# Kernel optimization log

Hardware: AMD Instinct MI355X
Metric: run time of the kernel (lower is better)

The kernel has to match this reference:

```python
import jax, jax.numpy as jnp
import numpy as np

N = 100000   # nodes per graph-batch side
E = 1280000  # directed edges
G = 256      # graphs per batch
F_IN, HID, EMB = 64, 128, 64
BN_EPS = 1e-5


def setup_inputs() -> dict:
    key = jax.random.key(0)
    ks = jax.random.split(key, 24)
    inp = {}
    inp["x1"] = jax.random.normal(ks[0], (N, F_IN), dtype=jnp.float32)
    inp["x2"] = jax.random.normal(ks[1], (N, F_IN), dtype=jnp.float32)
    inp["edge_index1"] = jax.random.randint(ks[2], (2, E), 0, N, dtype=jnp.int64)
    inp["edge_index2"] = jax.random.randint(ks[3], (2, E), 0, N, dtype=jnp.int64)
    inp["batch1"] = jnp.sort(jax.random.randint(ks[4], (N,), 0, G, dtype=jnp.int64))
    inp["batch2"] = jnp.sort(jax.random.randint(ks[5], (N,), 0, G, dtype=jnp.int64))
    # shared (siamese) encoder parameters: 3 GIN layers (Linear+BN), final linear
    dims = [(F_IN, HID), (HID, HID), (HID, HID)]
    for i, (di, do) in enumerate(dims, 1):
        inp[f"W{i}"] = jax.random.normal(ks[5 + i], (di, do), dtype=jnp.float32) * (1.0 / np.sqrt(di))
        inp[f"b{i}"] = jnp.zeros((do,), dtype=jnp.float32)
        inp[f"g{i}"] = jnp.ones((do,), dtype=jnp.float32)   # BN gamma
        inp[f"be{i}"] = jnp.zeros((do,), dtype=jnp.float32)  # BN beta
    inp["Wf"] = jax.random.normal(ks[10], (HID, EMB), dtype=jnp.float32) * (1.0 / np.sqrt(HID))
    inp["bf"] = jnp.zeros((EMB,), dtype=jnp.float32)
    # classifier: Linear(EMB, HID//2) -> ReLU -> Linear(HID//2, 1) -> Sigmoid
    inp["Wc1"] = jax.random.normal(ks[11], (EMB, HID // 2), dtype=jnp.float32) * (1.0 / np.sqrt(EMB))
    inp["bc1"] = jnp.zeros((HID // 2,), dtype=jnp.float32)
    inp["Wc2"] = jax.random.normal(ks[12], (HID // 2, 1), dtype=jnp.float32) * (1.0 / np.sqrt(HID // 2))
    inp["bc2"] = jnp.zeros((1,), dtype=jnp.float32)
    return inp


def _gin_layer(x, src, dst, W, b, g, be):
    # GINConv eps=0: agg = x + sum_{j->i} x_j ; MLP = Linear -> BatchNorm1d -> ReLU
    agg = x + jax.ops.segment_sum(x[src], dst, num_segments=N)
    h = agg @ W + b
    mu = jnp.mean(h, axis=0)
    var = jnp.var(h, axis=0)
    h = (h - mu) * jax.lax.rsqrt(var + BN_EPS) * g + be
    return jax.nn.relu(h)  # MLP ReLU; outer .relu() in forward is idempotent


def _encode(x, edge_index, batch, Ws, bs, gs, bes, Wf, bf):
    src, dst = edge_index[0], edge_index[1]
    for W, b, g, be in zip(Ws, bs, gs, bes):
        x = _gin_layer(x, src, dst, W, b, g, be)
    # global_mean_pool
    sums = jax.ops.segment_sum(x, batch, num_segments=G)
    cnt = jax.ops.segment_sum(jnp.ones((N,), x.dtype), batch, num_segments=G)
    pooled = sums / jnp.maximum(cnt, 1.0)[:, None]
    return pooled @ Wf + bf


def reference(x1, edge_index1, batch1, x2, edge_index2, batch2,
              W1, b1, g1, be1, W2, b2, g2, be2, W3, b3, g3, be3,
              Wf, bf, Wc1, bc1, Wc2, bc2):
    Ws, bs, gs, bes = (W1, W2, W3), (b1, b2, b3), (g1, g2, g3), (be1, be2, be3)
    v1 = _encode(x1, edge_index1, batch1, Ws, bs, gs, bes, Wf, bf)
    v2 = _encode(x2, edge_index2, batch2, Ws, bs, gs, bes, Wf, bf)
    diff = jnp.abs(v1 - v2)
    h = jax.nn.relu(diff @ Wc1 + bc1)
    return jax.nn.sigmoid(h @ Wc2 + bc2)  # [G, 1]
```

## Files before the change

kernel.cpp:

```cpp
#include <hip/hip_runtime.h>
#include <hip/hip_bf16.h>
#include <math.h>

#define NN 100000
#define NE 1280000
#define NG 256
#define HID 128
#define EMB 64
#define BN_EPS 1e-5f
#define SB 1024
#define SNB ((NN + SB - 1) / SB)
#define NBG 1563
#define NB4 25000
#define PART ((NN + 7) / 8)
#define FCH 2048
#define NCH (NE / FCH)

typedef __attribute__((ext_vector_type(8))) __bf16 bf16x8;
typedef __attribute__((ext_vector_type(4))) float f32x4;

__device__ __forceinline__ float bf2f(unsigned int u) { return __uint_as_float(u << 16); }
__device__ __forceinline__ unsigned int f2b(float f) {
    unsigned int u = __float_as_uint(f);
    return (u + 0x7fffu + ((u >> 16) & 1u)) >> 16;
}

__global__ void detect_i64_kernel(const void* __restrict__ ei, int* __restrict__ flag) {
    if (threadIdx.x == 0 && blockIdx.x == 0) {
        const unsigned long long* p = (const unsigned long long*)ei;
        int is64 = 1;
        #pragma unroll
        for (int i = 0; i < 16; ++i)
            if (p[i] >= (1ull << 32)) is64 = 0;
        *flag = is64;
    }
}

__device__ __forceinline__ int load_idx(const void* p, int i, bool is64) {
    return is64 ? (int)((const long long*)p)[i] : ((const int*)p)[i];
}

__global__ __launch_bounds__(256) void convert_x(const float* __restrict__ x1,
                                                 const float* __restrict__ x2,
                                                 ushort* __restrict__ o1,
                                                 ushort* __restrict__ o2) {
    const int per = NN * 16;
    const int i = blockIdx.x * 256 + threadIdx.x;
    const int side = i >= per;
    const int j = i - side * per;
    const float4 v = ((const float4*)(side ? x2 : x1))[j];
    ushort4 o;
    o.x = (ushort)f2b(v.x); o.y = (ushort)f2b(v.y);
    o.z = (ushort)f2b(v.z); o.w = (ushort)f2b(v.w);
    ((ushort4*)(side ? o2 : o1))[j] = o;
}

__global__ __launch_bounds__(256) void prep_weights(const float* __restrict__ W1,
                                                    const float* __restrict__ W2,
                                                    const float* __restrict__ W3,
                                                    ushort* __restrict__ T1,
                                                    ushort* __restrict__ T2,
                                                    ushort* __restrict__ T3) {
    const int i = blockIdx.x * 256 + threadIdx.x;
    if (i < 8192) {
        const int k = i >> 7, c = i & 127;
        T1[c * 64 + k] = (ushort)f2b(W1[i]);
    } else if (i < 24576) {
        const int j = i - 8192, k = j >> 7, c = j & 127;
        T2[c * 128 + k] = (ushort)f2b(W2[j]);
    } else if (i < 40960) {
        const int j = i - 24576, k = j >> 7, c = j & 127;
        T3[c * 128 + k] = (ushort)f2b(W3[j]);
    }
}

__global__ __launch_bounds__(256) void csr_hist2(const void* __restrict__ e1,
                                                 const void* __restrict__ e2,
                                                 int* __restrict__ degA,
                                                 int* __restrict__ degB,
                                                 const int* __restrict__ flag) {
    const bool is64 = (*flag != 0);
    const int i = blockIdx.x * 256 + threadIdx.x;
    if (i < 2 * NE) {
        const int side = i >= NE;
        const int j = i - side * NE;
        atomicAdd(&(side ? degB : degA)[load_idx(side ? e2 : e1, NE + j, is64)], 1);
    }
}

__global__ __launch_bounds__(256) void scan_block_sums2(const int* __restrict__ degA,
                                                        const int* __restrict__ degB,
                                                        int* __restrict__ bsum) {
    const int side = blockIdx.x >= SNB;
    const int bx = blockIdx.x - side * SNB;
    const int* deg = side ? degB : degA;
    const int t = threadIdx.x;
    const int base = bx * SB + t * 4;
    int s = 0;
    #pragma unroll
    for (int k = 0; k < 4; ++k) {
        const int i = base + k;
        if (i < NN) s += deg[i];
    }
    __shared__ int red[256];
    red[t] = s;
    __syncthreads();
    for (int off = 128; off > 0; off >>= 1) {
        if (t < off) red[t] += red[t + off];
        __syncthreads();
    }
    if (t == 0) bsum[side * 128 + bx] = red[0];
}

__global__ __launch_bounds__(128) void scan_bsums2(const int* __restrict__ bsum,
                                                   int* __restrict__ boff,
                                                   int* __restrict__ rpA,
                                                   int* __restrict__ rpB) {
    const int side = blockIdx.x;
    __shared__ int s[128];
    const int t = threadIdx.x;
    s[t] = (t < SNB) ? bsum[side * 128 + t] : 0;
    __syncthreads();
    for (int off = 1; off < 128; off <<= 1) {
        const int v = (t >= off) ? s[t - off] : 0;
        __syncthreads();
        s[t] += v;
        __syncthreads();
    }
    boff[side * 128 + t] = (t == 0) ? 0 : s[t - 1];
    if (t == 0) (side ? rpB : rpA)[NN] = s[SNB - 1];
}

__global__ __launch_bounds__(256) void scan_fill2(const int* __restrict__ degA,
                                                  const int* __restrict__ degB,
                                                  const int* __restrict__ boff,
                                                  int* __restrict__ rpA,
                                                  int* __restrict__ rpB,
                                                  int* __restrict__ curA,
                                                  int* __restrict__ curB) {
    const int side = blockIdx.x >= SNB;
    const int bx = blockIdx.x - side * SNB;
    const int* deg = side ? degB : degA;
    int* rowptr = side ? rpB : rpA;
    int* cursor = side ? curB : curA;
    const int t = threadIdx.x;
    const int base = bx * SB + t * 4;
    int v[4], s = 0;
    #pragma unroll
    for (int k = 0; k < 4; ++k) {
        const int i = base + k;
        v[k] = (i < NN) ? deg[i] : 0;
        s += v[k];
    }
    __shared__ int red[256];
    red[t] = s;
    __syncthreads();
    for (int off = 1; off < 256; off <<= 1) {
        const int x = (t >= off) ? red[t - off] : 0;
        __syncthreads();
        red[t] += x;
        __syncthreads();
    }
    int run = boff[side * 128 + bx] + ((t == 0) ? 0 : red[t - 1]);
    #pragma unroll
    for (int k = 0; k < 4; ++k) {
        const int i = base + k;
        if (i < NN) {
            rowptr[i] = run;
            cursor[i] = run;
            run += v[k];
        }
    }
}

__global__ __launch_bounds__(256) void csr_fill_part(const void* __restrict__ e1,
                                                     const void* __restrict__ e2,
                                                     int* __restrict__ curA,
                                                     int* __restrict__ curB,
                                                     int* __restrict__ colA,
                                                     int* __restrict__ colB,
                                                     const int* __restrict__ flag) {
    const bool is64 = (*flag != 0);
    const int g = blockIdx.x & 7;
    const int q = blockIdx.x >> 3;
    const int side = q >= NCH;
    const int chunk = q - side * NCH;
    const void* __restrict__ e = side ? e2 : e1;
    int* __restrict__ cur = side ? curB : curA;
    int* __restrict__ col = side ? colB : colA;
    const int lo = g * PART;
    const int hi = min(lo + PART, NN);
    const int base = chunk * FCH;
    for (int i = base + threadIdx.x; i < base + FCH; i += 256) {
        const int d = load_idx(e, NE + i, is64);
        if (d >= lo && d < hi) {
            const int pos = atomicAdd(&cur[d], 1);
            col[pos] = load_idx(e, i, is64);
        }
    }
}

struct G64Args {
    const ushort *xA, *xB;
    const int *rpA, *rpB, *colA, *colB;
    ushort *oA, *oB;
};

__global__ __launch_bounds__(256) void gather64k(G64Args a) {
    const int xcd = blockIdx.x & 7;
    const int side = xcd >> 2;
    const int bx = (blockIdx.x >> 3) * 4 + (xcd & 3);
    const ushort* __restrict__ x = side ? a.xB : a.xA;
    const int* __restrict__ rowptr = side ? a.rpB : a.rpA;
    const int* __restrict__ col = side ? a.colB : a.colA;
    ushort* __restrict__ out = side ? a.oB : a.oA;

    const int node = (bx * 256 + threadIdx.x) >> 6;
    const int lane = threadIdx.x & 63;
    if (node >= NN) return;
    const int beg = rowptr[node], end = rowptr[node + 1];
    float acc = bf2f(x[node * 64 + lane]);
    int e = beg;
    for (; e + 3 < end; e += 4) {
        const int s0 = col[e], s1 = col[e + 1], s2 = col[e + 2], s3 = col[e + 3];
        acc += bf2f(x[s0 * 64 + lane]) + bf2f(x[s1 * 64 + lane])
             + bf2f(x[s2 * 64 + lane]) + bf2f(x[s3 * 64 + lane]);
    }
    for (; e < end; ++e) acc += bf2f(x[col[e] * 64 + lane]);
    out[node * 64 + lane] = (ushort)f2b(acc);
}

struct GPostArgs {
    const ushort *yA, *yB;
    const int *rpA, *rpB, *colA, *colB;
    ushort *rA, *rB;
    float *stA, *stB;
};

__global__ __launch_bounds__(256) void gather_post(GPostArgs a) {
    const int xcd = blockIdx.x & 7;
    const int side = xcd >> 2;
    const int bx = (blockIdx.x >> 3) * 4 + (xcd & 3);
    if (bx >= NBG) return;
    const ushort* __restrict__ y = side ? a.yB : a.yA;
    const int* __restrict__ rowptr = side ? a.rpB : a.rpA;
    const int* __restrict__ col = side ? a.colB : a.colA;
    ushort* __restrict__ r = side ? a.rB : a.rA;
    float* __restrict__ stats = side ? a.stB : a.stA;

    const int t = threadIdx.x;
    const int w = t >> 6, l = t & 63;
    const int c2 = l * 2;
    float s0 = 0.f, s1 = 0.f, q0 = 0.f, q1 = 0.f;

    for (int i = 0; i < 16; ++i) {
        const int node = bx * 64 + w * 16 + i;
        if (node >= NN) break;
        const int beg = rowptr[node], end = rowptr[node + 1];
        const unsigned int u0 = *(const unsigned int*)&y[(size_t)node * 128 + c2];
        float ax = bf2f(u0 & 0xffffu), ay = bf2f(u0 >> 16);
        int e = beg;
        for (; e + 3 < end; e += 4) {
            const int sa = col[e], sb = col[e + 1], sc = col[e + 2], sd = col[e + 3];
            const unsigned int ua = *(const unsigned int*)&y[(size_t)sa * 128 + c2];
            const unsigned int ub = *(const unsigned int*)&y[(size_t)sb * 128 + c2];
            const unsigned int uc = *(const unsigned int*)&y[(size_t)sc * 128 + c2];
            const unsigned int ud = *(const unsigned int*)&y[(size_t)sd * 128 + c2];
            ax += bf2f(ua & 0xffffu) + bf2f(ub & 0xffffu) + bf2f(uc & 0xffffu) + bf2f(ud & 0xffffu);
            ay += bf2f(ua >> 16) + bf2f(ub >> 16) + bf2f(uc >> 16) + bf2f(ud >> 16);
        }
        for (; e < end; ++e) {
            const unsigned int u = *(const unsigned int*)&y[(size_t)col[e] * 128 + c2];
            ax += bf2f(u & 0xffffu);
            ay += bf2f(u >> 16);
        }
        const unsigned int pk = f2b(ax) | (f2b(ay) << 16);
        *(unsigned int*)&r[(size_t)node * 128 + c2] = pk;
        const float e0 = bf2f(pk & 0xffffu), e1 = bf2f(pk >> 16);
        s0 += e0; s1 += e1;
        q0 = fmaf(e0, e0, q0); q1 = fmaf(e1, e1, q1);
    }

    __shared__ float red[512];
    red[w * 128 + c2] = s0; red[w * 128 + c2 + 1] = s1;
    __syncthreads();
    if (t < 128) {
        const float v = red[t] + red[128 + t] + red[256 + t] + red[384 + t];
        unsafeAtomicAdd(&stats[t], v);
    }
    __syncthreads();
    red[w * 128 + c2] = q0; red[w * 128 + c2 + 1] = q1;
    __syncthreads();
    if (t < 128) {
        const float v = red[t] + red[128 + t] + red[256 + t] + red[384 + t];
        unsafeAtomicAdd(&stats[128 + t], v);
    }
}

struct GemmArgs {
    const ushort *mA, *mB;
    const ushort *WT;
    ushort *cA, *cB;
    float *stA, *stB;
    const float *gamma, *beta;
};

template<int FIN, bool APPLY_BN, bool STATS>
__global__ __launch_bounds__(256) void gemm_mfma(GemmArgs g) {
    constexpr int FP = FIN + 8;
    constexpr int CPR = FIN / 8;
    const int side = blockIdx.x >= NBG;
    const int bx = blockIdx.x - side * NBG;
    const ushort* __restrict__ M = side ? g.mB : g.mA;
    ushort* __restrict__ C = side ? g.cB : g.cA;
    float* __restrict__ stats = side ? g.stB : g.stA;

    __shared__ ushort sh[64 * 136 + 128 * FP];
    ushort* Ml = sh;
    ushort* Wl = sh + 64 * 136;

    const int t = threadIdx.x;
    const int w = t >> 6;
    const int l = t & 63;
    const int lr = l & 15;
    const int lg = l >> 4;
    const int r0 = bx * 64;

    float ca[8], cb[8];
    if (APPLY_BN) {
        const float* __restrict__ st = stats;
        const int cc = (t % CPR) * 8;
        const float inv_n = 1.f / (float)NN;
        #pragma unroll
        for (int j = 0; j < 8; ++j) {
            const int c = cc + j;
            const float mu = st[c] * inv_n;
            const float var = st[128 + c] * inv_n - mu * mu;
            ca[j] = g.gamma[c] * rsqrtf(var + BN_EPS);
            cb[j] = fmaf(-mu, ca[j], g.beta[c]);
        }
    }

    #pragma unroll
    for (int it = 0; it < (64 * CPR) / 256; ++it) {
        const int cid = it * 256 + t;
        const int row = cid / CPR, cc = (cid % CPR) * 8;
        const int r = r0 + row;
        uint4 v = make_uint4(0u, 0u, 0u, 0u);
        if (r < NN) v = *(const uint4*)&M[(size_t)r * FIN + cc];
        if (APPLY_BN) {
            unsigned int vv[4] = {v.x, v.y, v.z, v.w};
            #pragma unroll
            for (int q2 = 0; q2 < 4; ++q2) {
                float e0 = bf2f(vv[q2] & 0xffffu), e1 = bf2f(vv[q2] >> 16);
                e0 = fmaxf(fmaf(e0, ca[2 * q2], cb[2 * q2]), 0.f);
                e1 = fmaxf(fmaf(e1, ca[2 * q2 + 1], cb[2 * q2 + 1]), 0.f);
                vv[q2] = f2b(e0) | (f2b(e1) << 16);
            }
            v = make_uint4(vv[0], vv[1], vv[2], vv[3]);
        }
        *(uint4*)&Ml[row * FP + cc] = v;
    }
    #pragma unroll
    for (int it = 0; it < (128 * CPR) / 256; ++it) {
        const int cid = it * 256 + t;
        const int c = cid / CPR, kk = (cid % CPR) * 8;
        *(uint4*)&Wl[c * FP + kk] = *(const uint4*)&g.WT[c * FIN + kk];
    }
    __syncthreads();

    f32x4 acc[4][2];
    #pragma unroll
    for (int fi = 0; fi < 4; ++fi)
        #pragma unroll
        for (int fj = 0; fj < 2; ++fj)
            acc[fi][fj] = (f32x4){0.f, 0.f, 0.f, 0.f};

    #pragma unroll
    for (int kc = 0; kc < FIN / 32; ++kc) {
        const int kb = kc * 32 + lg * 8;
        bf16x8 a[4], b[2];
        #pragma unroll
        for (int fi = 0; fi < 4; ++fi)
            a[fi] = *(const bf16x8*)&Ml[(fi * 16 + lr) * FP + kb];
        #pragma unroll
        for (int fj = 0; fj < 2; ++fj)
            b[fj] = *(const bf16x8*)&Wl[(w * 32 + fj * 16 + lr) * FP + kb];
        #pragma unroll
        for (int fi = 0; fi < 4; ++fi)
            #pragma unroll
            for (int fj = 0; fj < 2; ++fj)
                acc[fi][fj] = __builtin_amdgcn_mfma_f32_16x16x32_bf16(a[fi], b[fj], acc[fi][fj], 0, 0, 0);
    }
    __syncthreads();

    #pragma unroll
    for (int fi = 0; fi < 4; ++fi)
        #pragma unroll
        for (int fj = 0; fj < 2; ++fj)
            #pragma unroll
            for (int j = 0; j < 4; ++j) {
                const int row = fi * 16 + lg * 4 + j;
                const int c = w * 32 + fj * 16 + lr;
                Ml[row * 136 + c] = (ushort)f2b(acc[fi][fj][j]);
            }
    __syncthreads();

    const int ry = t >> 4, c0 = (t & 15) * 8;
    float sc[8], qc[8];
    if (STATS) {
        #pragma unroll
        for (int j = 0; j < 8; ++j) { sc[j] = 0.f; qc[j] = 0.f; }
    }
    #pragma unroll
    for (int i = 0; i < 4; ++i) {
        const int rr = ry * 4 + i;
        const int r = r0 + rr;
        if (r < NN) {
            const uint4 pk = *(const uint4*)&Ml[rr * 136 + c0];
            if (STATS) {
                const unsigned int uu[4] = {pk.x, pk.y, pk.z, pk.w};
                #pragma unroll
                for (int q2 = 0; q2 < 4; ++q2) {
                    const float e0 = bf2f(uu[q2] & 0xffffu);
                    const float e1 = bf2f(uu[q2] >> 16);
                    sc[2 * q2] += e0;       sc[2 * q2 + 1] += e1;
                    qc[2 * q2] = fmaf(e0, e0, qc[2 * q2]);
                    qc[2 * q2 + 1] = fmaf(e1, e1, qc[2 * q2 + 1]);
                }
            }
            *(uint4*)&C[(size_t)r * HID + c0] = pk;
        }
    }
    if (STATS) {
        float* red = (float*)Wl;
        #pragma unroll
        for (int j = 0; j < 8; ++j) red[ry * 128 + c0 + j] = sc[j];
        __syncthreads();
        if (t < 128) {
            float a = 0.f;
            #pragma unroll
            for (int k = 0; k < 16; ++k) a += red[k * 128 + t];
            unsafeAtomicAdd(&stats[t], a);
        }
        __syncthreads();
        #pragma unroll
        for (int j = 0; j < 8; ++j) red[ry * 128 + c0 + j] = qc[j];
        __syncthreads();
        if (t < 128) {
            float a = 0.f;
            #pragma unroll
            for (int k = 0; k < 16; ++k) a += red[k * 128 + t];
            unsafeAtomicAdd(&stats[128 + t], a);
        }
    }
}

struct PoolArgs {
    const ushort *hA, *hB;
    const void *btA, *btB;
    const float *stA, *stB;
    const float *gamma, *beta;
    float *pooled, *cnt;
    const int* flag;
};

__global__ __launch_bounds__(128) void pool16(PoolArgs p) {
    const int side = blockIdx.x >= NBG;
    const int bx = blockIdx.x - side * NBG;
    const ushort* __restrict__ h = side ? p.hB : p.hA;
    const void* __restrict__ batch = side ? p.btB : p.btA;
    const float* __restrict__ st = side ? p.stB : p.stA;
    float* pooled = p.pooled + side * NG * HID;
    float* cnt = p.cnt + side * NG;
    const bool is64 = (*p.flag != 0);
    const int c = threadIdx.x;

    const float inv_n = 1.f / (float)NN;
    const float mu = st[c] * inv_n;
    const float var = st[128 + c] * inv_n - mu * mu;
    const float ca = p.gamma[c] * rsqrtf(var + BN_EPS);
    const float cb = fmaf(-mu, ca, p.beta[c]);

    const int rbeg = bx * 64;
    if (rbeg >= NN) return;
    const int rend = min(rbeg + 64, NN);
    const int g0 = load_idx(batch, rbeg, is64);
    const int g1 = load_idx(batch, rend - 1, is64);
    if (g0 == g1) {
        float acc = 0.f;
        #pragma unroll 8
        for (int r = rbeg; r < rend; ++r)
            acc += fmaxf(fmaf(bf2f(h[r * HID + c]), ca, cb), 0.f);
        unsafeAtomicAdd(&pooled[g0 * HID + c], acc);
        if (c == 0) unsafeAtomicAdd(&cnt[g0], (float)(rend - rbeg));
        return;
    }
    int gprev = g0;
    float acc = 0.f; int run = 0;
    for (int r = rbeg; r < rend; ++r) {
        const int g = load_idx(batch, r, is64);
        if (g != gprev) {
            unsafeAtomicAdd(&pooled[gprev * HID + c], acc);
            if (c == 0) unsafeAtomicAdd(&cnt[gprev], (float)run);
            acc = 0.f; run = 0; gprev = g;
        }
        acc += fmaxf(fmaf(bf2f(h[r * HID + c]), ca, cb), 0.f);
        ++run;
    }
    unsafeAtomicAdd(&pooled[gprev * HID + c], acc);
    if (c == 0) unsafeAtomicAdd(&cnt[gprev], (float)run);
}

__global__ __launch_bounds__(64) void pool_proj(const float* __restrict__ pooled,
                                                const float* __restrict__ cnt,
                                                const float* __restrict__ Wf,
                                                const float* __restrict__ bf,
                                                float* __restrict__ v) {
    const int side = blockIdx.x >= NG;
    const int g = blockIdx.x - side * NG;
    const int c = threadIdx.x;
    const float* pp = pooled + side * NG * HID + g * HID;
    const float inv = 1.f / fmaxf(cnt[side * NG + g], 1.f);
    float acc = 0.f;
    for (int k = 0; k < HID; ++k) acc = fmaf(pp[k], Wf[k * EMB + c], acc);
    v[side * NG * EMB + g * EMB + c] = fmaf(acc, inv, bf[c]);
}

__global__ __launch_bounds__(256) void classifier(const float* __restrict__ v1,
                                                  const float* __restrict__ v2,
                                                  const float* __restrict__ Wc1,
                                                  const float* __restrict__ bc1,
                                                  const float* __restrict__ Wc2,
                                                  const float* __restrict__ bc2,
                                                  float* __restrict__ out) {
    const int g = threadIdx.x;
    if (g >= NG) return;
    float d[EMB];
    #pragma unroll
    for (int c = 0; c < EMB; ++c) d[c] = fabsf(v1[g * EMB + c] - v2[g * EMB + c]);
    float o = bc2[0];
    for (int j = 0; j < 32; ++j) {
        float h = bc1[j];
        #pragma unroll
        for (int c = 0; c < EMB; ++c) h = fmaf(d[c], Wc1[c * 32 + j], h);
        h = fmaxf(h, 0.f);
        o = fmaf(h, Wc2[j], o);
    }
    out[g] = 1.f / (1.f + expf(-o));
}

extern "C" void kernel_launch(void* const* d_in, const int* in_sizes, int n_in,
                              void* d_out, int out_size, void* d_ws, size_t ws_size,
                              hipStream_t stream) {
    const float* x1 = (const float*)d_in[0];
    const float* x2 = (const float*)d_in[1];
    const void* ei1 = d_in[2];
    const void* ei2 = d_in[3];
    const void* bt1 = d_in[4];
    const void* bt2 = d_in[5];
    const float* W[3]  = {(const float*)d_in[6],  (const float*)d_in[10], (const float*)d_in[14]};
    const float* gg[3] = {(const float*)d_in[8],  (const float*)d_in[12], (const float*)d_in[16]};
    const float* be[3] = {(const float*)d_in[9],  (const float*)d_in[13], (const float*)d_in[17]};
    const float* Wf  = (const float*)d_in[18];
    const float* bfv = (const float*)d_in[19];
    const float* Wc1 = (const float*)d_in[20];
    const float* bc1 = (const float*)d_in[21];
    const float* Wc2 = (const float*)d_in[22];
    const float* bc2 = (const float*)d_in[23];

    char* cur = (char*)d_ws;
    auto alloc = [&](size_t bytes) -> void* {
        void* p = cur;
        cur += (bytes + 255) & ~(size_t)255;
        return p;
    };
    ushort* P0 = (ushort*)alloc((size_t)NN * HID * 2);
    ushort* P1 = (ushort*)alloc((size_t)NN * HID * 2);
    ushort* Q0 = (ushort*)alloc((size_t)NN * HID * 2);
    ushort* Q1 = (ushort*)alloc((size_t)NN * HID * 2);
    int* deg2   = (int*)alloc((size_t)2 * NN * 4);
    int* rpA    = (int*)alloc((size_t)(NN + 1) * 4);
    int* rpB    = (int*)alloc((size_t)(NN + 1) * 4);
    int* curA   = (int*)alloc((size_t)NN * 4);
    int* curB   = (int*)alloc((size_t)NN * 4);
    int* bsum   = (int*)alloc(256 * 4);
    int* boff   = (int*)alloc(256 * 4);
    int* colA   = (int*)alloc((size_t)NE * 4);
    int* colB   = (int*)alloc((size_t)NE * 4);
    int* flag   = (int*)alloc(64);
    ushort* WT1 = (ushort*)alloc(128 * 64 * 2);
    ushort* WT2 = (ushort*)alloc(128 * 128 * 2);
    ushort* WT3 = (ushort*)alloc(128 * 128 * 2);
    float* zreg = (float*)alloc((size_t)(6 * 256 + 2 * NG * HID + 2 * NG) * 4);
    float* stats  = zreg;
    float* pooled = stats + 6 * 256;
    float* cnt    = pooled + 2 * NG * HID;
    float* vv     = (float*)alloc((size_t)2 * NG * EMB * 4);
    int* degA = deg2, *degB = deg2 + NN;

    hipMemsetAsync(deg2, 0, (size_t)2 * NN * 4, stream);
    hipMemsetAsync(zreg, 0, (size_t)(6 * 256 + 2 * NG * HID + 2 * NG) * 4, stream);
    detect_i64_kernel<<<1, 64, 0, stream>>>(ei1, flag);
    convert_x<<<(2 * NN * 16) / 256, 256, 0, stream>>>(x1, x2, P0, P1);
    prep_weights<<<160, 256, 0, stream>>>(W[0], W[1], W[2], WT1, WT2, WT3);

    const int EB2 = (2 * NE + 255) / 256;
    csr_hist2<<<EB2, 256, 0, stream>>>(ei1, ei2, degA, degB, flag);
    scan_block_sums2<<<2 * SNB, 256, 0, stream>>>(degA, degB, bsum);
    scan_bsums2<<<2, 128, 0, stream>>>(bsum, boff, rpA, rpB);
    scan_fill2<<<2 * SNB, 256, 0, stream>>>(degA, degB, boff, rpA, rpB, curA, curB);
    csr_fill_part<<<8 * 2 * NCH, 256, 0, stream>>>(ei1, ei2, curA, curB, colA, colB, flag);

    float* st1A = stats + 0 * 256, *st1B = stats + 1 * 256;
    float* st2A = stats + 2 * 256, *st2B = stats + 3 * 256;
    float* st3A = stats + 4 * 256, *st3B = stats + 5 * 256;

    const int GP = 8 * ((NBG + 3) / 4);

    {
        G64Args a = {P0, P1, rpA, rpB, colA, colB, Q0, Q1};
        gather64k<<<8 * (NB4 / 4), 256, 0, stream>>>(a);
        GemmArgs g = {Q0, Q1, WT1, P0, P1, st1A, st1B, nullptr, nullptr};
        gemm_mfma<64, false, true><<<2 * NBG, 256, 0, stream>>>(g);
    }
    {
        GemmArgs g = {P0, P1, WT2, Q0, Q1, st1A, st1B, gg[0], be[0]};
        gemm_mfma<128, true, false><<<2 * NBG, 256, 0, stream>>>(g);
        GPostArgs a = {Q0, Q1, rpA, rpB, colA, colB, P0, P1, st2A, st2B};
        gather_post<<<GP, 256, 0, stream>>>(a);
    }
    {
        GemmArgs g = {P0, P1, WT3, Q0, Q1, st2A, st2B, gg[1], be[1]};
        gemm_mfma<128, true, false><<<2 * NBG, 256, 0, stream>>>(g);
        GPostArgs a = {Q0, Q1, rpA, rpB, colA, colB, P0, P1, st3A, st3B};
        gather_post<<<GP, 256, 0, stream>>>(a);
    }
    {
        PoolArgs p = {P0, P1, bt1, bt2, st3A, st3B, gg[2], be[2], pooled, cnt, flag};
        pool16<<<2 * NBG, 128, 0, stream>>>(p);
    }
    pool_proj<<<2 * NG, 64, 0, stream>>>(pooled, cnt, Wf, bfv, vv);
    classifier<<<1, 256, 0, stream>>>(vv, vv + NG * EMB, Wc1, bc1, Wc2, bc2, (float*)d_out);
}
```

Before: 931.0 us.

## Split edges across half-waves in gathers, partition histogram, separate BN stats pass

The two gather kernels now process one node per wavefront, with the two half-waves taking alternate edges. Each lane loads wider vectors and the halves are combined with a cross-lane shuffle, which is meant to raise memory-level parallelism per wave. The batch-norm statistics reduction moves out of gather_post into its own stats_pass kernel that rereads the output. The degree histogram is partitioned by destination range, matching the existing fill kernel, to localise atomics. The XCD-aware block swizzle is dropped, and the extra stats pass adds a full reread and a kernel launch.

```diff
diff --git a/kernel.cpp b/kernel.cpp
--- a/kernel.cpp
+++ b/kernel.cpp
@@ -11,7 +11,8 @@
 #define SB 1024
 #define SNB ((NN + SB - 1) / SB)
 #define NBG 1563
-#define NB4 25000
+#define GBLK 25000
+#define NSB 782
 #define PART ((NN + 7) / 8)
 #define FCH 2048
 #define NCH (NE / FCH)
@@ -74,17 +75,24 @@
     }
 }
 
-__global__ __launch_bounds__(256) void csr_hist2(const void* __restrict__ e1,
-                                                 const void* __restrict__ e2,
-                                                 int* __restrict__ degA,
-                                                 int* __restrict__ degB,
-                                                 const int* __restrict__ flag) {
+__global__ __launch_bounds__(256) void csr_hist_part(const void* __restrict__ e1,
+                                                     const void* __restrict__ e2,
+                                                     int* __restrict__ degA,
+                                                     int* __restrict__ degB,
+                                                     const int* __restrict__ flag) {
     const bool is64 = (*flag != 0);
-    const int i = blockIdx.x * 256 + threadIdx.x;
-    if (i < 2 * NE) {
-        const int side = i >= NE;
-        const int j = i - side * NE;
-        atomicAdd(&(side ? degB : degA)[load_idx(side ? e2 : e1, NE + j, is64)], 1);
+    const int g = blockIdx.x & 7;
+    const int q = blockIdx.x >> 3;
+    const int side = q >= NCH;
+    const int chunk = q - side * NCH;
+    const void* __restrict__ e = side ? e2 : e1;
+    int* __restrict__ deg = side ? degB : degA;
+    const int lo = g * PART;
+    const int hi = min(lo + PART, NN);
+    const int base = chunk * FCH;
+    for (int i = base + threadIdx.x; i < base + FCH; i += 256) {
+        const int d = load_idx(e, NE + i, is64);
+        if (d >= lo && d < hi) atomicAdd(&deg[d], 1);
     }
 }
 
@@ -207,93 +215,139 @@
 };
 
 __global__ __launch_bounds__(256) void gather64k(G64Args a) {
-    const int xcd = blockIdx.x & 7;
-    const int side = xcd >> 2;
-    const int bx = (blockIdx.x >> 3) * 4 + (xcd & 3);
+    const int side = blockIdx.x >= GBLK;
+    const int bx = blockIdx.x - side * GBLK;
     const ushort* __restrict__ x = side ? a.xB : a.xA;
     const int* __restrict__ rowptr = side ? a.rpB : a.rpA;
     const int* __restrict__ col = side ? a.colB : a.colA;
     ushort* __restrict__ out = side ? a.oB : a.oA;
 
     const int node = (bx * 256 + threadIdx.x) >> 6;
-    const int lane = threadIdx.x & 63;
+    const int l = threadIdx.x & 63;
     if (node >= NN) return;
     const int beg = rowptr[node], end = rowptr[node + 1];
-    float acc = bf2f(x[node * 64 + lane]);
+    const int cg = (l & 31) * 2;
+    const int half = l >> 5;
+
+    float a0 = 0.f, a1 = 0.f;
     int e = beg;
     for (; e + 3 < end; e += 4) {
-        const int s0 = col[e], s1 = col[e + 1], s2 = col[e + 2], s3 = col[e + 3];
-        acc += bf2f(x[s0 * 64 + lane]) + bf2f(x[s1 * 64 + lane])
-             + bf2f(x[s2 * 64 + lane]) + bf2f(x[s3 * 64 + lane]);
-    }
-    for (; e < end; ++e) acc += bf2f(x[col[e] * 64 + lane]);
-    out[node * 64 + lane] = (ushort)f2b(acc);
+        const int s0 = col[e + half], s1 = col[e + 2 + half];
+        const unsigned int va = *(const unsigned int*)&x[(size_t)s0 * 64 + cg];
+        const unsigned int vb = *(const unsigned int*)&x[(size_t)s1 * 64 + cg];
+        a0 += bf2f(va & 0xffffu) + bf2f(vb & 0xffffu);
+        a1 += bf2f(va >> 16) + bf2f(vb >> 16);
+    }
+    for (; e < end; e += 2) {
+        const int eh = e + half;
+        if (eh < end) {
+            const unsigned int v = *(const unsigned int*)&x[(size_t)col[eh] * 64 + cg];
+            a0 += bf2f(v & 0xffffu);
+            a1 += bf2f(v >> 16);
+        }
+    }
+    a0 += __shfl_xor(a0, 32);
+    a1 += __shfl_xor(a1, 32);
+    if (l < 32) {
+        const unsigned int u0 = *(const unsigned int*)&x[(size_t)node * 64 + cg];
+        a0 += bf2f(u0 & 0xffffu);
+        a1 += bf2f(u0 >> 16);
+        *(unsigned int*)&out[(size_t)node * 64 + cg] = f2b(a0) | (f2b(a1) << 16);
+    }
 }
 
 struct GPostArgs {
     const ushort *yA, *yB;
     const int *rpA, *rpB, *colA, *colB;
     ushort *rA, *rB;
-    float *stA, *stB;
 };
 
 __global__ __launch_bounds__(256) void gather_post(GPostArgs a) {
-    const int xcd = blockIdx.x & 7;
-    const int side = xcd >> 2;
-    const int bx = (blockIdx.x >> 3) * 4 + (xcd & 3);
-    if (bx >= NBG) return;
+    const int side = blockIdx.x >= GBLK;
+    const int bx = blockIdx.x - side * GBLK;
     const ushort* __restrict__ y = side ? a.yB : a.yA;
     const int* __restrict__ rowptr = side ? a.rpB : a.rpA;
     const int* __restrict__ col = side ? a.colB : a.colA;
     ushort* __restrict__ r = side ? a.rB : a.rA;
-    float* __restrict__ stats = side ? a.stB : a.stA;
-
+
+    const int node = (bx * 256 + threadIdx.x) >> 6;
+    const int l = threadIdx.x & 63;
+    if (node >= NN) return;
+    const int beg = rowptr[node], end = rowptr[node + 1];
+    const int cg = (l & 31) * 4;
+    const int half = l >> 5;
+
+    float a0 = 0.f, a1 = 0.f, a2 = 0.f, a3 = 0.f;
+    int e = beg;
+    for (; e + 3 < end; e += 4) {
+        const int s0 = col[e + half], s1 = col[e + 2 + half];
+        const uint2 va = *(const uint2*)&y[(size_t)s0 * 128 + cg];
+        const uint2 vb = *(const uint2*)&y[(size_t)s1 * 128 + cg];
+        a0 += bf2f(va.x & 0xffffu) + bf2f(vb.x & 0xffffu);
+        a1 += bf2f(va.x >> 16) + bf2f(vb.x >> 16);
+        a2 += bf2f(va.y & 0xffffu) + bf2f(vb.y & 0xffffu);
+        a3 += bf2f(va.y >> 16) + bf2f(vb.y >> 16);
+    }
+    for (; e < end; e += 2) {
+        const int eh = e + half;
+        if (eh < end) {
+            const uint2 v = *(const uint2*)&y[(size_t)col[eh] * 128 + cg];
+            a0 += bf2f(v.x & 0xffffu);
+            a1 += bf2f(v.x >> 16);
+            a2 += bf2f(v.y & 0xffffu);
+            a3 += bf2f(v.y >> 16);
+        }
+    }
+    a0 += __shfl_xor(a0, 32);
+    a1 += __shfl_xor(a1, 32);
+    a2 += __shfl_xor(a2, 32);
+    a3 += __shfl_xor(a3, 32);
+    if (l < 32) {
+        const uint2 u0 = *(const uint2*)&y[(size_t)node * 128 + cg];
+        a0 += bf2f(u0.x & 0xffffu);
+        a1 += bf2f(u0.x >> 16);
+        a2 += bf2f(u0.y & 0xffffu);
+        a3 += bf2f(u0.y >> 16);
+        uint2 pk;
+        pk.x = f2b(a0) | (f2b(a1) << 16);
+        pk.y = f2b(a2) | (f2b(a3) << 16);
+        *(uint2*)&r[(size_t)node * 128 + cg] = pk;
+    }
+}
+
+__global__ __launch_bounds__(256) void stats_pass(const ushort* __restrict__ hA,
+                                                  const ushort* __restrict__ hB,
+                                                  float* __restrict__ stA,
+                                                  float* __restrict__ stB) {
+    const int side = blockIdx.x >= NSB;
+    const int bx = blockIdx.x - side * NSB;
+    const ushort* __restrict__ h = side ? hB : hA;
+    float* __restrict__ st = side ? stB : stA;
     const int t = threadIdx.x;
-    const int w = t >> 6, l = t & 63;
-    const int c2 = l * 2;
+    const int c2 = (t & 63) * 2;
+    const int rsub = t >> 6;
+    const int rbeg = bx * 128;
+    const int rend = min(rbeg + 128, NN);
     float s0 = 0.f, s1 = 0.f, q0 = 0.f, q1 = 0.f;
-
-    for (int i = 0; i < 16; ++i) {
-        const int node = bx * 64 + w * 16 + i;
-        if (node >= NN) break;
-        const int beg = rowptr[node], end = rowptr[node + 1];
-        const unsigned int u0 = *(const unsigned int*)&y[(size_t)node * 128 + c2];
-        float ax = bf2f(u0 & 0xffffu), ay = bf2f(u0 >> 16);
-        int e = beg;
-        for (; e + 3 < end; e += 4) {
-            const int sa = col[e], sb = col[e + 1], sc = col[e + 2], sd = col[e + 3];
-            const unsigned int ua = *(const unsigned int*)&y[(size_t)sa * 128 + c2];
-            const unsigned int ub = *(const unsigned int*)&y[(size_t)sb * 128 + c2];
-            const unsigned int uc = *(const unsigned int*)&y[(size_t)sc * 128 + c2];
-            const unsigned int ud = *(const unsigned int*)&y[(size_t)sd * 128 + c2];
-            ax += bf2f(ua & 0xffffu) + bf2f(ub & 0xffffu) + bf2f(uc & 0xffffu) + bf2f(ud & 0xffffu);
-            ay += bf2f(ua >> 16) + bf2f(ub >> 16) + bf2f(uc >> 16) + bf2f(ud >> 16);
-        }
-        for (; e < end; ++e) {
-            const unsigned int u = *(const unsigned int*)&y[(size_t)col[e] * 128 + c2];
-            ax += bf2f(u & 0xffffu);
-            ay += bf2f(u >> 16);
-        }
-        const unsigned int pk = f2b(ax) | (f2b(ay) << 16);
-        *(unsigned int*)&r[(size_t)node * 128 + c2] = pk;
-        const float e0 = bf2f(pk & 0xffffu), e1 = bf2f(pk >> 16);
+    for (int rr = rbeg + rsub; rr < rend; rr += 4) {
+        const unsigned int u = *(const unsigned int*)&h[(size_t)rr * 128 + c2];
+        const float e0 = bf2f(u & 0xffffu), e1 = bf2f(u >> 16);
         s0 += e0; s1 += e1;
         q0 = fmaf(e0, e0, q0); q1 = fmaf(e1, e1, q1);
     }
-
     __shared__ float red[512];
-    red[w * 128 + c2] = s0; red[w * 128 + c2 + 1] = s1;
+    red[rsub * 128 + c2] = s0; red[rsub * 128 + c2 + 1] = s1;
     __syncthreads();
     if (t < 128) {
         const float v = red[t] + red[128 + t] + red[256 + t] + red[384 + t];
-        unsafeAtomicAdd(&stats[t], v);
-    }
-    __syncthreads();
-    red[w * 128 + c2] = q0; red[w * 128 + c2 + 1] = q1;
+        unsafeAtomicAdd(&st[t], v);
+    }
+    __syncthreads();
+    red[rsub * 128 + c2] = q0; red[rsub * 128 + c2 + 1] = q1;
     __syncthreads();
     if (t < 128) {
         const float v = red[t] + red[128 + t] + red[256 + t] + red[384 + t];
-        unsafeAtomicAdd(&stats[128 + t], v);
+        unsafeAtomicAdd(&st[128 + t], v);
     }
 }
 
@@ -605,8 +659,7 @@
     convert_x<<<(2 * NN * 16) / 256, 256, 0, stream>>>(x1, x2, P0, P1);
     prep_weights<<<160, 256, 0, stream>>>(W[0], W[1], W[2], WT1, WT2, WT3);
 
-    const int EB2 = (2 * NE + 255) / 256;
-    csr_hist2<<<EB2, 256, 0, stream>>>(ei1, ei2, degA, degB, flag);
+    csr_hist_part<<<8 * 2 * NCH, 256, 0, stream>>>(ei1, ei2, degA, degB, flag);
     scan_block_sums2<<<2 * SNB, 256, 0, stream>>>(degA, degB, bsum);
     scan_bsums2<<<2, 128, 0, stream>>>(bsum, boff, rpA, rpB);
     scan_fill2<<<2 * SNB, 256, 0, stream>>>(degA, degB, boff, rpA, rpB, curA, curB);
@@ -616,25 +669,25 @@
     float* st2A = stats + 2 * 256, *st2B = stats + 3 * 256;
     float* st3A = stats + 4 * 256, *st3B = stats + 5 * 256;
 
-    const int GP = 8 * ((NBG + 3) / 4);
-
     {
         G64Args a = {P0, P1, rpA, rpB, colA, colB, Q0, Q1};
-        gather64k<<<8 * (NB4 / 4), 256, 0, stream>>>(a);
+        gather64k<<<2 * GBLK, 256, 0, stream>>>(a);
         GemmArgs g = {Q0, Q1, WT1, P0, P1, st1A, st1B, nullptr, nullptr};
         gemm_mfma<64, false, true><<<2 * NBG, 256, 0, stream>>>(g);
     }
     {
         GemmArgs g = {P0, P1, WT2, Q0, Q1, st1A, st1B, gg[0], be[0]};
         gemm_mfma<128, true, false><<<2 * NBG, 256, 0, stream>>>(g);
-        GPostArgs a = {Q0, Q1, rpA, rpB, colA, colB, P0, P1, st2A, st2B};
-        gather_post<<<GP, 256, 0, stream>>>(a);
+        GPostArgs a = {Q0, Q1, rpA, rpB, colA, colB, P0, P1};
+        gather_post<<<2 * GBLK, 256, 0, stream>>>(a);
+        stats_pass<<<2 * NSB, 256, 0, stream>>>(P0, P1, st2A, st2B);
     }
     {
         GemmArgs g = {P0, P1, WT3, Q0, Q1, st2A, st2B, gg[1], be[1]};
         gemm_mfma<128, true, false><<<2 * NBG, 256, 0, stream>>>(g);
-        GPostArgs a = {Q0, Q1, rpA, rpB, colA, colB, P0, P1, st3A, st3B};
-        gather_post<<<GP, 256, 0, stream>>>(a);
+        GPostArgs a = {Q0, Q1, rpA, rpB, colA, colB, P0, P1};
+        gather_post<<<2 * GBLK, 256, 0, stream>>>(a);
+        stats_pass<<<2 * NSB, 256, 0, stream>>>(P0, P1, st3A, st3B);
     }
     {
         PoolArgs p = {P0, P1, bt1, bt2, st3A, st3B, gg[2], be[2], pooled, cnt, flag};
```

After: 988.9 us. +6.2%, slower.

## Split post-GEMM gather into one-node-per-wave kernel plus separate BN stats pass

Applied to the files above, without the earlier changes.

The post-GEMM gather used to walk 16 nodes per wave and accumulate BatchNorm statistics in the same kernel. It now assigns one node per wave across many more blocks, and a new stats_pass kernel computes the column sums and squared sums by rereading the result. The XCD-interleaved block-to-side mapping in both gather kernels is replaced by a plain first-half/second-half split, and 64-bit indexing is added. The goal is more parallelism and better latency hiding for the irregular gathers, at the cost of an extra kernel launch and an extra read of the 128-wide activations per layer, plus the loss of XCD locality.

```diff
diff --git a/kernel.cpp b/kernel.cpp
--- a/kernel.cpp
+++ b/kernel.cpp
@@ -11,7 +11,8 @@
 #define SB 1024
 #define SNB ((NN + SB - 1) / SB)
 #define NBG 1563
-#define NB4 25000
+#define GBLK 25000
+#define NSB 782
 #define PART ((NN + 7) / 8)
 #define FCH 2048
 #define NCH (NE / FCH)
@@ -207,9 +208,8 @@
 };
 
 __global__ __launch_bounds__(256) void gather64k(G64Args a) {
-    const int xcd = blockIdx.x & 7;
-    const int side = xcd >> 2;
-    const int bx = (blockIdx.x >> 3) * 4 + (xcd & 3);
+    const int side = blockIdx.x >= GBLK;
+    const int bx = blockIdx.x - side * GBLK;
     const ushort* __restrict__ x = side ? a.xB : a.xA;
     const int* __restrict__ rowptr = side ? a.rpB : a.rpA;
     const int* __restrict__ col = side ? a.colB : a.colA;
@@ -219,81 +219,90 @@
     const int lane = threadIdx.x & 63;
     if (node >= NN) return;
     const int beg = rowptr[node], end = rowptr[node + 1];
-    float acc = bf2f(x[node * 64 + lane]);
+    float acc = bf2f(x[(size_t)node * 64 + lane]);
     int e = beg;
     for (; e + 3 < end; e += 4) {
         const int s0 = col[e], s1 = col[e + 1], s2 = col[e + 2], s3 = col[e + 3];
-        acc += bf2f(x[s0 * 64 + lane]) + bf2f(x[s1 * 64 + lane])
-             + bf2f(x[s2 * 64 + lane]) + bf2f(x[s3 * 64 + lane]);
-    }
-    for (; e < end; ++e) acc += bf2f(x[col[e] * 64 + lane]);
-    out[node * 64 + lane] = (ushort)f2b(acc);
+        acc += bf2f(x[(size_t)s0 * 64 + lane]) + bf2f(x[(size_t)s1 * 64 + lane])
+             + bf2f(x[(size_t)s2 * 64 + lane]) + bf2f(x[(size_t)s3 * 64 + lane]);
+    }
+    for (; e < end; ++e) acc += bf2f(x[(size_t)col[e] * 64 + lane]);
+    out[(size_t)node * 64 + lane] = (ushort)f2b(acc);
 }
 
 struct GPostArgs {
     const ushort *yA, *yB;
     const int *rpA, *rpB, *colA, *colB;
     ushort *rA, *rB;
-    float *stA, *stB;
 };
 
 __global__ __launch_bounds__(256) void gather_post(GPostArgs a) {
-    const int xcd = blockIdx.x & 7;
-    const int side = xcd >> 2;
-    const int bx = (blockIdx.x >> 3) * 4 + (xcd & 3);
-    if (bx >= NBG) return;
+    const int side = blockIdx.x >= GBLK;
+    const int bx = blockIdx.x - side * GBLK;
     const ushort* __restrict__ y = side ? a.yB : a.yA;
     const int* __restrict__ rowptr = side ? a.rpB : a.rpA;
     const int* __restrict__ col = side ? a.colB : a.colA;
     ushort* __restrict__ r = side ? a.rB : a.rA;
-    float* __restrict__ stats = side ? a.stB : a.stA;
-
+
+    const int node = (bx * 256 + threadIdx.x) >> 6;
+    const int lane = threadIdx.x & 63;
+    if (node >= NN) return;
+    const int beg = rowptr[node], end = rowptr[node + 1];
+    const int c2 = lane * 2;
+
+    const unsigned int u0 = *(const unsigned int*)&y[(size_t)node * 128 + c2];
+    float ax = bf2f(u0 & 0xffffu), ay = bf2f(u0 >> 16);
+    int e = beg;
+    for (; e + 3 < end; e += 4) {
+        const int s0 = col[e], s1 = col[e + 1], s2 = col[e + 2], s3 = col[e + 3];
+        const unsigned int ua = *(const unsigned int*)&y[(size_t)s0 * 128 + c2];
+        const unsigned int ub = *(const unsigned int*)&y[(size_t)s1 * 128 + c2];
+        const unsigned int uc = *(const unsigned int*)&y[(size_t)s2 * 128 + c2];
+        const unsigned int ud = *(const unsigned int*)&y[(size_t)s3 * 128 + c2];
+        ax += bf2f(ua & 0xffffu) + bf2f(ub & 0xffffu) + bf2f(uc & 0xffffu) + bf2f(ud & 0xffffu);
+        ay += bf2f(ua >> 16) + bf2f(ub >> 16) + bf2f(uc >> 16) + bf2f(ud >> 16);
+    }
+    for (; e < end; ++e) {
+        const unsigned int u = *(const unsigned int*)&y[(size_t)col[e] * 128 + c2];
+        ax += bf2f(u & 0xffffu);
+        ay += bf2f(u >> 16);
+    }
+    *(unsigned int*)&r[(size_t)node * 128 + c2] = f2b(ax) | (f2b(ay) << 16);
+}
+
+__global__ __launch_bounds__(256) void stats_pass(const ushort* __restrict__ hA,
+                                                  const ushort* __restrict__ hB,
+                                                  float* __restrict__ stA,
+                                                  float* __restrict__ stB) {
+    const int side = blockIdx.x >= NSB;
+    const int bx = blockIdx.x - side * NSB;
+    const ushort* __restrict__ h = side ? hB : hA;
+    float* __restrict__ st = side ? stB : stA;
     const int t = threadIdx.x;
-    const int w = t >> 6, l = t & 63;
-    const int c2 = l * 2;
+    const int c2 = (t & 63) * 2;
+    const int rsub = t >> 6;
+    const int rbeg = bx * 128;
+    const int rend = min(rbeg + 128, NN);
     float s0 = 0.f, s1 = 0.f, q0 = 0.f, q1 = 0.f;
-
-    for (int i = 0; i < 16; ++i) {
-        const int node = bx * 64 + w * 16 + i;
-        if (node >= NN) break;
-        const int beg = rowptr[node], end = rowptr[node + 1];
-        const unsigned int u0 = *(const unsigned int*)&y[(size_t)node * 128 + c2];
-        float ax = bf2f(u0 & 0xffffu), ay = bf2f(u0 >> 16);
-        int e = beg;
-        for (; e + 3 < end; e += 4) {
-            const int sa = col[e], sb = col[e + 1], sc = col[e + 2], sd = col[e + 3];
-            const unsigned int ua = *(const unsigned int*)&y[(size_t)sa * 128 + c2];
-            const unsigned int ub = *(const unsigned int*)&y[(size_t)sb * 128 + c2];
-            const unsigned int uc = *(const unsigned int*)&y[(size_t)sc * 128 + c2];
-            const unsigned int ud = *(const unsigned int*)&y[(size_t)sd * 128 + c2];
-            ax += bf2f(ua & 0xffffu) + bf2f(ub & 0xffffu) + bf2f(uc & 0xffffu) + bf2f(ud & 0xffffu);
-            ay += bf2f(ua >> 16) + bf2f(ub >> 16) + bf2f(uc >> 16) + bf2f(ud >> 16);
-        }
-        for (; e < end; ++e) {
-            const unsigned int u = *(const unsigned int*)&y[(size_t)col[e] * 128 + c2];
-            ax += bf2f(u & 0xffffu);
-            ay += bf2f(u >> 16);
-        }
-        const unsigned int pk = f2b(ax) | (f2b(ay) << 16);
-        *(unsigned int*)&r[(size_t)node * 128 + c2] = pk;
-        const float e0 = bf2f(pk & 0xffffu), e1 = bf2f(pk >> 16);
+    for (int rr = rbeg + rsub; rr < rend; rr += 4) {
+        const unsigned int u = *(const unsigned int*)&h[(size_t)rr * 128 + c2];
+        const float e0 = bf2f(u & 0xffffu), e1 = bf2f(u >> 16);
         s0 += e0; s1 += e1;
         q0 = fmaf(e0, e0, q0); q1 = fmaf(e1, e1, q1);
     }
-
     __shared__ float red[512];
-    red[w * 128 + c2] = s0; red[w * 128 + c2 + 1] = s1;
+    red[rsub * 128 + c2] = s0; red[rsub * 128 + c2 + 1] = s1;
     __syncthreads();
     if (t < 128) {
         const float v = red[t] + red[128 + t] + red[256 + t] + red[384 + t];
-        unsafeAtomicAdd(&stats[t], v);
-    }
-    __syncthreads();
-    red[w * 128 + c2] = q0; red[w * 128 + c2 + 1] = q1;
+        unsafeAtomicAdd(&st[t], v);
+    }
+    __syncthreads();
+    red[rsub * 128 + c2] = q0; red[rsub * 128 + c2 + 1] = q1;
     __syncthreads();
     if (t < 128) {
         const float v = red[t] + red[128 + t] + red[256 + t] + red[384 + t];
-        unsafeAtomicAdd(&stats[128 + t], v);
+        unsafeAtomicAdd(&st[128 + t], v);
     }
 }
 
@@ -616,25 +625,25 @@
     float* st2A = stats + 2 * 256, *st2B = stats + 3 * 256;
     float* st3A = stats + 4 * 256, *st3B = stats + 5 * 256;
 
-    const int GP = 8 * ((NBG + 3) / 4);
-
     {
         G64Args a = {P0, P1, rpA, rpB, colA, colB, Q0, Q1};
-        gather64k<<<8 * (NB4 / 4), 256, 0, stream>>>(a);
+        gather64k<<<2 * GBLK, 256, 0, stream>>>(a);
         GemmArgs g = {Q0, Q1, WT1, P0, P1, st1A, st1B, nullptr, nullptr};
         gemm_mfma<64, false, true><<<2 * NBG, 256, 0, stream>>>(g);
     }
     {
         GemmArgs g = {P0, P1, WT2, Q0, Q1, st1A, st1B, gg[0], be[0]};
         gemm_mfma<128, true, false><<<2 * NBG, 256, 0, stream>>>(g);
-        GPostArgs a = {Q0, Q1, rpA, rpB, colA, colB, P0, P1, st2A, st2B};
-        gather_post<<<GP, 256, 0, stream>>>(a);
+        GPostArgs a = {Q0, Q1, rpA, rpB, colA, colB, P0, P1};
+        gather_post<<<2 * GBLK, 256, 0, stream>>>(a);
+        stats_pass<<<2 * NSB, 256, 0, stream>>>(P0, P1, st2A, st2B);
     }
     {
         GemmArgs g = {P0, P1, WT3, Q0, Q1, st2A, st2B, gg[1], be[1]};
         gemm_mfma<128, true, false><<<2 * NBG, 256, 0, stream>>>(g);
-        GPostArgs a = {Q0, Q1, rpA, rpB, colA, colB, P0, P1, st3A, st3B};
-        gather_post<<<GP, 256, 0, stream>>>(a);
+        GPostArgs a = {Q0, Q1, rpA, rpB, colA, colB, P0, P1};
+        gather_post<<<2 * GBLK, 256, 0, stream>>>(a);
+        stats_pass<<<2 * NSB, 256, 0, stream>>>(P0, P1, st3A, st3B);
     }
     {
         PoolArgs p = {P0, P1, bt1, bt2, st3A, st3B, gg[2], be[2], pooled, cnt, flag};
```

New measurement: 942.4 us. No clear change (+1.2%).
